# Kernel tuning notes

Hardware: AMD Instinct MI355X
Metric: run time of the kernel (lower is better)

The kernel has to match this reference:

```python
import jax, jax.numpy as jnp
import numpy as np

SEQ = 2048
D_MODEL = 1024
N_HEADS = 16
TOP_K = 64
Q_LR = 128
KV_LR = 128
ROPE_DIM = 32
V_DIM = 64
IDX_DIM = 64
# Mamba2 indexer block: expand=1, headdim=32, d_state=64, d_conv=4
D_INNER = D_MODEL
M_HD = 32
M_NH = D_INNER // M_HD  # 32 ssm heads
M_DS = 64
M_DC = 4
CONV_CH = D_INNER + 2 * M_DS  # 1152
IN_DIM = 2 * D_INNER + 2 * M_DS + M_NH  # 2208


def _silu(x):
    return x * jax.nn.sigmoid(x)


def _mamba2(x, in_w, conv_w, conv_b, dt_bias, A_log, D, norm_w, out_w):
    # Minimal Mamba2 (SSD) recurrent forward: in_proj -> causal depthwise conv
    # on (x, B, C) -> selective scan with scalar-per-head A -> gated RMSNorm -> out_proj.
    L = x.shape[0]
    zxbcdt = x @ in_w.T  # [L, IN_DIM]
    z = zxbcdt[:, :D_INNER]
    xBC = zxbcdt[:, D_INNER:D_INNER + CONV_CH]
    dt = zxbcdt[:, -M_NH:]
    # causal depthwise conv1d, kernel M_DC
    xp = jnp.pad(xBC, ((M_DC - 1, 0), (0, 0)))
    conv = conv_b
    for k in range(M_DC):
        conv = conv + xp[k:k + L] * conv_w[:, k]
    xBC = _silu(conv)
    xs = xBC[:, :D_INNER].reshape(L, M_NH, M_HD)          # [L,h,p]
    B = xBC[:, D_INNER:D_INNER + M_DS]                     # [L,n]
    C = xBC[:, D_INNER + M_DS:]                            # [L,n]
    dt = jax.nn.softplus(dt + dt_bias)                     # [L,h]
    dA = jnp.exp(dt * (-jnp.exp(A_log)))                   # [L,h]
    dBx = jnp.einsum('lh,lhp,ln->lhpn', dt, xs, B)         # [L,h,p,n]

    def step(h, inp):
        dA_t, dBx_t, C_t = inp
        h = h * dA_t[:, None, None] + dBx_t
        y_t = jnp.einsum('hpn,n->hp', h, C_t)
        return h, y_t

    h0 = jnp.zeros((M_NH, M_HD, M_DS), x.dtype)
    _, y = jax.lax.scan(step, h0, (dA, dBx, C))            # y: [L,h,p]
    y = y + D[:, None] * xs
    y = y.reshape(L, D_INNER) * _silu(z)                   # gated
    y = y * jax.lax.rsqrt(jnp.mean(y * y, axis=-1, keepdims=True) + 1e-5) * norm_w
    return y @ out_w.T


def _make_rope(L):
    inv = 1.0 / (10000.0 ** (jnp.arange(0, ROPE_DIM, 2, dtype=jnp.float32) / ROPE_DIM))
    ang = jnp.arange(L, dtype=jnp.float32)[:, None] * inv  # [L, ROPE/2]
    return jnp.sin(ang), jnp.cos(ang)


def _apply_rope(x, sin, cos):
    # x: [L, H, ROPE_DIM]; rotate-half convention
    x1, x2 = jnp.split(x, 2, axis=-1)
    s = sin[:, None, :]
    c = cos[:, None, :]
    return jnp.concatenate([x1 * c - x2 * s, x1 * s + x2 * c], axis=-1)


def _forward(x, idx_in_w, idx_conv_w, idx_conv_b, idx_dt_bias, idx_A_log, idx_D,
             idx_norm_w, idx_out_w, idx_q_w, idx_k_w, q_down_w, q_up_w, q_rope_w,
             kv_down_w, kv_up_w, k_rope_w, out_w):
    L = x.shape[0]
    # --- Mamba2 indexer scores ---
    x_mamba = _mamba2(x, idx_in_w, idx_conv_w, idx_conv_b, idx_dt_bias,
                      idx_A_log, idx_D, idx_norm_w, idx_out_w)
    q_idx = x_mamba @ idx_q_w.T                            # [L, IDX_DIM]
    k_idx = x @ idx_k_w.T                                  # [L, IDX_DIM]
    scores = (q_idx @ k_idx.T) * (IDX_DIM ** -0.5)         # [L, L]
    mask = jnp.tril(jnp.ones((L, L), dtype=bool))
    scores = jnp.where(mask, scores, -jnp.inf)
    k_val = min(TOP_K, L)
    _, indices = jax.lax.top_k(scores, k_val)              # [L, K]
    # --- MLA low-rank projections ---
    c_q = x @ q_down_w.T                                   # [L, Q_LR]
    q_content = (c_q @ q_up_w.T).reshape(L, N_HEADS, V_DIM)
    q_rope = (c_q @ q_rope_w.T).reshape(L, N_HEADS, ROPE_DIM)
    c_kv = x @ kv_down_w.T                                 # [L, KV_LR]
    kv = c_kv @ kv_up_w.T                                  # [L, 2*H*V]
    k_content_flat, v_flat = jnp.split(kv, 2, axis=-1)
    k_content = k_content_flat.reshape(L, N_HEADS, V_DIM)
    v = v_flat.reshape(L, N_HEADS, V_DIM)
    k_rope_shared = (x @ k_rope_w.T)[:, None, :]           # [L, 1, ROPE]
    sin, cos = _make_rope(L)
    q_rope_rot = _apply_rope(q_rope, sin, cos)
    k_rope_rot = jnp.tile(_apply_rope(k_rope_shared, sin, cos), (1, N_HEADS, 1))
    q_final = jnp.concatenate([q_content, q_rope_rot], axis=-1)  # [L,H,dk]
    k_final = jnp.concatenate([k_content, k_rope_rot], axis=-1)  # [L,H,dk]
    # --- top-k gather sparse attention ---
    k_sparse = k_final[indices]                            # [L,K,H,dk]
    v_sparse = v[indices]                                  # [L,K,H,dv]
    dk = k_final.shape[-1]
    logits = jnp.einsum('lhd,lkhd->lhk', q_final, k_sparse) * (dk ** -0.5)
    w = jax.nn.softmax(logits, axis=-1)
    attn = jnp.einsum('lhk,lkhd->lhd', w, v_sparse).reshape(L, N_HEADS * V_DIM)
    return attn @ out_w.T


def setup_inputs() -> dict:
    key = jax.random.key(0)
    ks = jax.random.split(key, 16)

    def g(k, shape, s=0.02):
        return jax.random.normal(k, shape, jnp.float32) * s

    return {
        "x": jax.random.normal(ks[0], (SEQ, D_MODEL), jnp.float32),
        "idx_in_w": g(ks[1], (IN_DIM, D_MODEL)),
        "idx_conv_w": g(ks[2], (CONV_CH, M_DC), 0.2),
        "idx_conv_b": jnp.zeros((CONV_CH,), jnp.float32),
        "idx_dt_bias": g(ks[3], (M_NH,), 0.1),
        "idx_A_log": jnp.log(jnp.arange(1, M_NH + 1, dtype=jnp.float32)),
        "idx_D": jnp.ones((M_NH,), jnp.float32),
        "idx_norm_w": jnp.ones((D_INNER,), jnp.float32),
        "idx_out_w": g(ks[4], (D_MODEL, D_INNER)),
        "idx_q_w": g(ks[5], (IDX_DIM, D_MODEL)),
        "idx_k_w": g(ks[6], (IDX_DIM, D_MODEL)),
        "q_down_w": g(ks[7], (Q_LR, D_MODEL)),
        "q_up_w": g(ks[8], (N_HEADS * V_DIM, Q_LR)),
        "q_rope_w": g(ks[9], (N_HEADS * ROPE_DIM, Q_LR)),
        "kv_down_w": g(ks[10], (KV_LR, D_MODEL)),
        "kv_up_w": g(ks[11], (2 * N_HEADS * V_DIM, KV_LR)),
        "k_rope_w": g(ks[12], (ROPE_DIM, D_MODEL)),
        "out_w": g(ks[13], (D_MODEL, N_HEADS * V_DIM)),
    }


def reference(x, idx_in_w, idx_conv_w, idx_conv_b, idx_dt_bias, idx_A_log, idx_D,
              idx_norm_w, idx_out_w, idx_q_w, idx_k_w, q_down_w, q_up_w, q_rope_w,
              kv_down_w, kv_up_w, k_rope_w, out_w):
    return _forward(x, idx_in_w, idx_conv_w, idx_conv_b, idx_dt_bias, idx_A_log,
                    idx_D, idx_norm_w, idx_out_w, idx_q_w, idx_k_w, q_down_w,
                    q_up_w, q_rope_w, kv_down_w, kv_up_w, k_rope_w, out_w)
```

## Files before the change

### kernel.cpp

```cpp
#include <hip/hip_runtime.h>
#include <math.h>

constexpr int L      = 2048;
constexpr int NH     = 16;
constexpr int DINNER = 1024;
constexpr int MNH    = 32;
constexpr int CONVCH = 1152;
constexpr int INDIMP = 2304;
constexpr int CHUNK  = 64;
constexpr int NCH    = 32;

using bf16x8 = __attribute__((ext_vector_type(8))) short;
using f32x4  = __attribute__((ext_vector_type(4))) float;

__device__ __forceinline__ f32x4 splat4(float x) { return (f32x4){x, x, x, x}; }

__device__ __forceinline__ unsigned short f2bf(float f) {
  unsigned u = __float_as_uint(f);
  return (unsigned short)((u + 0x7fffu + ((u >> 16) & 1u)) >> 16);
}
__device__ __forceinline__ float bf2f(unsigned short h) {
  return __uint_as_float((unsigned)h << 16);
}

__global__ __launch_bounds__(256) void gemm_f32_v3(
    const float* __restrict__ A, const float* __restrict__ W,
    float* __restrict__ C, int M, int N, int K, int tri) {
  __shared__ float As[16][132];
  __shared__ float Ws[16][132];
  int tid = threadIdx.x;
  int bm = blockIdx.y * 128, bn = blockIdx.x * 128;
  if (tri && bn > bm + 127) return;
  int kper = K / gridDim.z;
  int kb = blockIdx.z * kper, ke = kb + kper;
  int lr = tid >> 1;
  int lh = (tid & 1) * 8;
  int tx = tid & 15, ty = tid >> 4;
  bool wok = (bn + lr < N);
  const float* arow = A + (size_t)(bm + lr) * K + lh;
  const float* wrow = W + (size_t)(bn + lr) * K + lh;
  float4 a0, a1, w0, w1;
  auto gload = [&](int k0) {
    a0 = *(const float4*)(arow + k0);
    a1 = *(const float4*)(arow + k0 + 4);
    w0 = make_float4(0.f, 0.f, 0.f, 0.f); w1 = w0;
    if (wok) {
      w0 = *(const float4*)(wrow + k0);
      w1 = *(const float4*)(wrow + k0 + 4);
    }
  };
  f32x4 acc0[8] = {}, acc1[8] = {};
  gload(kb);
  for (int k0 = kb; k0 < ke; k0 += 16) {
    __syncthreads();
    As[lh+0][lr]=a0.x; As[lh+1][lr]=a0.y; As[lh+2][lr]=a0.z; As[lh+3][lr]=a0.w;
    As[lh+4][lr]=a1.x; As[lh+5][lr]=a1.y; As[lh+6][lr]=a1.z; As[lh+7][lr]=a1.w;
    Ws[lh+0][lr]=w0.x; Ws[lh+1][lr]=w0.y; Ws[lh+2][lr]=w0.z; Ws[lh+3][lr]=w0.w;
    Ws[lh+4][lr]=w1.x; Ws[lh+5][lr]=w1.y; Ws[lh+6][lr]=w1.z; Ws[lh+7][lr]=w1.w;
    __syncthreads();
    if (k0 + 16 < ke) gload(k0 + 16);
#pragma unroll
    for (int kk = 0; kk < 16; ++kk) {
      f32x4 b0 = *(const f32x4*)&Ws[kk][tx * 4];
      f32x4 b1 = *(const f32x4*)&Ws[kk][64 + tx * 4];
      f32x4 al = *(const f32x4*)&As[kk][ty * 8];
      f32x4 ah = *(const f32x4*)&As[kk][ty * 8 + 4];
#pragma unroll
      for (int i = 0; i < 4; ++i) {
        acc0[i]     += splat4(al[i]) * b0;
        acc1[i]     += splat4(al[i]) * b1;
        acc0[i + 4] += splat4(ah[i]) * b0;
        acc1[i + 4] += splat4(ah[i]) * b1;
      }
    }
  }
  bool single = (gridDim.z == 1);
#pragma unroll
  for (int i = 0; i < 8; ++i) {
    int row = bm + ty * 8 + i;
    float* crow = C + (size_t)row * N;
    int c0 = bn + tx * 4, c1 = bn + 64 + tx * 4;
    if (c0 + 3 < N) {
      if (single) *(f32x4*)(crow + c0) = acc0[i];
      else {
        atomicAdd(crow + c0 + 0, acc0[i][0]); atomicAdd(crow + c0 + 1, acc0[i][1]);
        atomicAdd(crow + c0 + 2, acc0[i][2]); atomicAdd(crow + c0 + 3, acc0[i][3]);
      }
    }
    if (c1 + 3 < N) {
      if (single) *(f32x4*)(crow + c1) = acc1[i];
      else {
        atomicAdd(crow + c1 + 0, acc1[i][0]); atomicAdd(crow + c1 + 1, acc1[i][1]);
        atomicAdd(crow + c1 + 2, acc1[i][2]); atomicAdd(crow + c1 + 3, acc1[i][3]);
      }
    }
  }
}

__global__ __launch_bounds__(256) void gemm_f32_dual(
    const float* __restrict__ A0, const float* __restrict__ W0, float* __restrict__ C0,
    const float* __restrict__ A1, const float* __restrict__ W1, float* __restrict__ C1,
    int M, int N, int K, int S) {
  __shared__ float As[16][132];
  __shared__ float Ws[16][132];
  int tid = threadIdx.x;
  int bm = blockIdx.y * 128, bn = blockIdx.x * 128;
  int pair = (int)blockIdx.z >= S;
  int zi = blockIdx.z - pair * S;
  const float* A = pair ? A1 : A0;
  const float* W = pair ? W1 : W0;
  float* C = pair ? C1 : C0;
  int kper = K / S;
  int kb = zi * kper, ke = kb + kper;
  int lr = tid >> 1;
  int lh = (tid & 1) * 8;
  int tx = tid & 15, ty = tid >> 4;
  bool wok = (bn + lr < N);
  const float* arow = A + (size_t)(bm + lr) * K + lh;
  const float* wrow = W + (size_t)(bn + lr) * K + lh;
  float4 a0, a1, w0, w1;
  auto gload = [&](int k0) {
    a0 = *(const float4*)(arow + k0);
    a1 = *(const float4*)(arow + k0 + 4);
    w0 = make_float4(0.f, 0.f, 0.f, 0.f); w1 = w0;
    if (wok) {
      w0 = *(const float4*)(wrow + k0);
      w1 = *(const float4*)(wrow + k0 + 4);
    }
  };
  f32x4 acc0[8] = {}, acc1[8] = {};
  gload(kb);
  for (int k0 = kb; k0 < ke; k0 += 16) {
    __syncthreads();
    As[lh+0][lr]=a0.x; As[lh+1][lr]=a0.y; As[lh+2][lr]=a0.z; As[lh+3][lr]=a0.w;
    As[lh+4][lr]=a1.x; As[lh+5][lr]=a1.y; As[lh+6][lr]=a1.z; As[lh+7][lr]=a1.w;
    Ws[lh+0][lr]=w0.x; Ws[lh+1][lr]=w0.y; Ws[lh+2][lr]=w0.z; Ws[lh+3][lr]=w0.w;
    Ws[lh+4][lr]=w1.x; Ws[lh+5][lr]=w1.y; Ws[lh+6][lr]=w1.z; Ws[lh+7][lr]=w1.w;
    __syncthreads();
    if (k0 + 16 < ke) gload(k0 + 16);
#pragma unroll
    for (int kk = 0; kk < 16; ++kk) {
      f32x4 b0 = *(const f32x4*)&Ws[kk][tx * 4];
      f32x4 b1 = *(const f32x4*)&Ws[kk][64 + tx * 4];
      f32x4 al = *(const f32x4*)&As[kk][ty * 8];
      f32x4 ah = *(const f32x4*)&As[kk][ty * 8 + 4];
#pragma unroll
      for (int i = 0; i < 4; ++i) {
        acc0[i]     += splat4(al[i]) * b0;
        acc1[i]     += splat4(al[i]) * b1;
        acc0[i + 4] += splat4(ah[i]) * b0;
        acc1[i + 4] += splat4(ah[i]) * b1;
      }
    }
  }
#pragma unroll
  for (int i = 0; i < 8; ++i) {
    int row = bm + ty * 8 + i;
    float* crow = C + (size_t)row * N;
    int c0 = bn + tx * 4, c1 = bn + 64 + tx * 4;
    if (c0 + 3 < N) {
      atomicAdd(crow + c0 + 0, acc0[i][0]); atomicAdd(crow + c0 + 1, acc0[i][1]);
      atomicAdd(crow + c0 + 2, acc0[i][2]); atomicAdd(crow + c0 + 3, acc0[i][3]);
    }
    if (c1 + 3 < N) {
      atomicAdd(crow + c1 + 0, acc1[i][0]); atomicAdd(crow + c1 + 1, acc1[i][1]);
      atomicAdd(crow + c1 + 2, acc1[i][2]); atomicAdd(crow + c1 + 3, acc1[i][3]);
    }
  }
}

__global__ __launch_bounds__(256) void transpose1024_kernel(
    const float* __restrict__ src, float* __restrict__ dst) {
  __shared__ float t[32][33];
  int bx = blockIdx.x & 31, by = blockIdx.x >> 5;
  int tx = threadIdx.x & 31, ty8 = threadIdx.x >> 5;
  for (int r = ty8; r < 32; r += 8)
    t[r][tx] = src[(size_t)(by * 32 + r) * 1024 + bx * 32 + tx];
  __syncthreads();
  for (int r = ty8; r < 32; r += 8)
    dst[(size_t)(bx * 32 + r) * 1024 + by * 32 + tx] = t[tx][r];
}

__global__ __launch_bounds__(256) void gemm_bf16_kernel(
    const unsigned short* __restrict__ A, const unsigned short* __restrict__ W,
    float* __restrict__ C, int M, int N, int K, int lda, int ldb, int ldc) {
  __shared__ unsigned short As[2][128 * 64];
  __shared__ unsigned short Ws[2][128 * 64];
  int tid = threadIdx.x;
  int bx = blockIdx.x, by = blockIdx.y;
  int nxy = gridDim.x * gridDim.y;
  if ((nxy & 7) == 0) {
    int lin = by * gridDim.x + bx;
    int cpx = nxy >> 3;
    int swz = (lin & 7) * cpx + (lin >> 3);
    bx = swz % gridDim.x;
    by = swz / gridDim.x;
  }
  int bm = by * 128, bn = bx * 128;
  int kper = K / gridDim.z;
  int k_begin = blockIdx.z * kper;
  int k_end = k_begin + kper;
  int wv = tid >> 6, lane = tid & 63;
  int wrow = (wv >> 1) * 64, wcol = (wv & 1) * 64;
  int lrow = lane & 15, quad = lane >> 4;

  f32x4 acc[4][4] = {};

  auto stage = [&](int b, int k0) {
#pragma unroll
    for (int it = 0; it < 4; ++it) {
      int s = it * 256 + tid;
      int r = s >> 3;
      int q = (s & 7) ^ (r & 7);
      const unsigned short* ga = A + (size_t)(bm + r) * lda + k0 + q * 8;
      const unsigned short* gw = W + (size_t)(bn + r) * ldb + k0 + q * 8;
      __builtin_amdgcn_global_load_lds((const __attribute__((address_space(1))) void*)ga,
                                       (__attribute__((address_space(3))) void*)&As[b][s * 8], 16, 0, 0);
      __builtin_amdgcn_global_load_lds((const __attribute__((address_space(1))) void*)gw,
                                       (__attribute__((address_space(3))) void*)&Ws[b][s * 8], 16, 0, 0);
    }
  };

  stage(0, k_begin);
  int cur = 0;
  for (int k0 = k_begin; k0 < k_end; k0 += 64) {
    __syncthreads();
    if (k0 + 64 < k_end) stage(cur ^ 1, k0 + 64);
#pragma unroll
    for (int ks = 0; ks < 2; ++ks) {
      bf16x8 af[4], wf[4];
#pragma unroll
      for (int i = 0; i < 4; ++i) {
        int ra = wrow + i * 16 + lrow;
        int qa = (ks * 4 + quad) ^ (ra & 7);
        af[i] = *(const bf16x8*)&As[cur][(ra * 8 + qa) * 8];
        int rw = wcol + i * 16 + lrow;
        int qw = (ks * 4 + quad) ^ (rw & 7);
        wf[i] = *(const bf16x8*)&Ws[cur][(rw * 8 + qw) * 8];
      }
#pragma unroll
      for (int i = 0; i < 4; ++i)
#pragma unroll
        for (int j = 0; j < 4; ++j)
          acc[i][j] = __builtin_amdgcn_mfma_f32_16x16x32_bf16(af[i], wf[j], acc[i][j], 0, 0, 0);
    }
    cur ^= 1;
  }
  bool single = (gridDim.z == 1);
#pragma unroll
  for (int i = 0; i < 4; ++i)
#pragma unroll
    for (int j = 0; j < 4; ++j)
#pragma unroll
      for (int r = 0; r < 4; ++r) {
        int row = bm + wrow + i * 16 + quad * 4 + r;
        int col = bn + wcol + j * 16 + lrow;
        float v = acc[i][j][r];
        if (single) C[(size_t)row * ldc + col] = v;
        else atomicAdd(&C[(size_t)row * ldc + col], v);
      }
}

__global__ __launch_bounds__(256) void gemm_bf16_dual(
    const unsigned short* __restrict__ A0, const unsigned short* __restrict__ W0,
    float* __restrict__ C0,
    const unsigned short* __restrict__ A1, const unsigned short* __restrict__ W1,
    float* __restrict__ C1,
    int nx0, int ldc0, int ldc1, int K, int ld) {
  __shared__ unsigned short As[2][128 * 64];
  __shared__ unsigned short Ws[2][128 * 64];
  int tid = threadIdx.x;
  int bx = blockIdx.x, by = blockIdx.y;
  int pair = bx >= nx0;
  int bxl = pair ? bx - nx0 : bx;
  const unsigned short* A = pair ? A1 : A0;
  const unsigned short* W = pair ? W1 : W0;
  float* C = pair ? C1 : C0;
  int ldc = pair ? ldc1 : ldc0;
  int bm = by * 128, bn = bxl * 128;
  int wv = tid >> 6, lane = tid & 63;
  int wrow = (wv >> 1) * 64, wcol = (wv & 1) * 64;
  int lrow = lane & 15, quad = lane >> 4;

  f32x4 acc[4][4] = {};

  auto stage = [&](int b, int k0) {
#pragma unroll
    for (int it = 0; it < 4; ++it) {
      int s = it * 256 + tid;
      int r = s >> 3;
      int q = (s & 7) ^ (r & 7);
      const unsigned short* ga = A + (size_t)(bm + r) * ld + k0 + q * 8;
      const unsigned short* gw = W + (size_t)(bn + r) * ld + k0 + q * 8;
      __builtin_amdgcn_global_load_lds((const __attribute__((address_space(1))) void*)ga,
                                       (__attribute__((address_space(3))) void*)&As[b][s * 8], 16, 0, 0);
      __builtin_amdgcn_global_load_lds((const __attribute__((address_space(1))) void*)gw,
                                       (__attribute__((address_space(3))) void*)&Ws[b][s * 8], 16, 0, 0);
    }
  };

  stage(0, 0);
  int cur = 0;
  for (int k0 = 0; k0 < K; k0 += 64) {
    __syncthreads();
    if (k0 + 64 < K) stage(cur ^ 1, k0 + 64);
#pragma unroll
    for (int ks = 0; ks < 2; ++ks) {
      bf16x8 af[4], wf[4];
#pragma unroll
      for (int i = 0; i < 4; ++i) {
        int ra = wrow + i * 16 + lrow;
        int qa = (ks * 4 + quad) ^ (ra & 7);
        af[i] = *(const bf16x8*)&As[cur][(ra * 8 + qa) * 8];
        int rw = wcol + i * 16 + lrow;
        int qw = (ks * 4 + quad) ^ (rw & 7);
        wf[i] = *(const bf16x8*)&Ws[cur][(rw * 8 + qw) * 8];
      }
#pragma unroll
      for (int i = 0; i < 4; ++i)
#pragma unroll
        for (int j = 0; j < 4; ++j)
          acc[i][j] = __builtin_amdgcn_mfma_f32_16x16x32_bf16(af[i], wf[j], acc[i][j], 0, 0, 0);
    }
    cur ^= 1;
  }
#pragma unroll
  for (int i = 0; i < 4; ++i)
#pragma unroll
    for (int j = 0; j < 4; ++j)
#pragma unroll
      for (int r = 0; r < 4; ++r) {
        int row = bm + wrow + i * 16 + quad * 4 + r;
        int col = bn + wcol + j * 16 + lrow;
        C[(size_t)row * ldc + col] = acc[i][j][r];
      }
}

__global__ __launch_bounds__(256) void prep_weights_kernel(
    const float* __restrict__ x, unsigned short* __restrict__ x_trip,
    const float* __restrict__ idx_in_w, unsigned short* __restrict__ w_in_trip,
    const float* __restrict__ q_down_w, const float* __restrict__ kv_down_w,
    const float* __restrict__ k_rope_w, unsigned short* __restrict__ w3down,
    const float* __restrict__ q_up_w, const float* __restrict__ q_rope_w,
    unsigned short* __restrict__ wqups,
    const float* __restrict__ kv_up_w, unsigned short* __restrict__ wkvup) {
  int i = blockIdx.x * 256 + threadIdx.x;
  if (i < 2097152) {
    float f = x[i];
    unsigned short h = f2bf(f);
    float r1 = f - bf2f(h);
    unsigned short m = f2bf(r1);
    unsigned short l = f2bf(r1 - bf2f(m));
    size_t o = (size_t)i * 6;
    x_trip[o] = h; x_trip[o + 1] = m; x_trip[o + 2] = l;
    x_trip[o + 3] = h; x_trip[o + 4] = m; x_trip[o + 5] = h;
  } else if (i < 4456448) {
    int j = i - 2097152;
    int n = j >> 10, k = j & 1023;
    unsigned short h = 0, m = 0, l = 0;
    if (n < 2208) {
      float f = idx_in_w[(size_t)n * 1024 + k];
      h = f2bf(f);
      float r1 = f - bf2f(h);
      m = f2bf(r1);
      l = f2bf(r1 - bf2f(m));
    }
    size_t o = (size_t)j * 6;
    w_in_trip[o] = h; w_in_trip[o + 1] = h; w_in_trip[o + 2] = h;
    w_in_trip[o + 3] = m; w_in_trip[o + 4] = m; w_in_trip[o + 5] = l;
  } else {
    int j2 = i - 4456448;
    const float* src; unsigned short* dst; int rows, K; size_t obase; int idx;
    if (j2 < 393216) {
      int r = j2 >> 17;
      idx = j2 & 131071;
      K = 1024;
      src = (r == 0) ? q_down_w : (r == 1) ? kv_down_w : k_rope_w;
      rows = (r == 2) ? 32 : 128;
      dst = w3down; obase = (size_t)(r * 131072 + idx) * 3;
    } else if (j2 < 524288) {
      idx = j2 - 393216; K = 128; src = q_up_w; rows = 1024;
      dst = wqups; obase = (size_t)idx * 3;
    } else if (j2 < 589824) {
      idx = j2 - 524288; K = 128; src = q_rope_w; rows = 512;
      dst = wqups; obase = (size_t)393216 + (size_t)idx * 3;
    } else {
      idx = j2 - 589824; K = 128; src = kv_up_w; rows = 2048;
      dst = wkvup; obase = (size_t)idx * 3;
    }
    int n = idx / K, k = idx - n * K;
    unsigned short hi = 0, lo = 0;
    if (n < rows) {
      float f = src[(size_t)n * K + k];
      hi = f2bf(f);
      lo = f2bf(f - bf2f(hi));
    }
    dst[obase] = hi; dst[obase + 1] = hi; dst[obase + 2] = lo;
  }
}

__global__ __launch_bounds__(256) void post_inproj_kernel(
    const float* __restrict__ out_w, unsigned short* __restrict__ w_outp,
    const float* __restrict__ zxbcdt, const float* __restrict__ conv_w,
    const float* __restrict__ conv_b, float* __restrict__ xBC,
    const float* __restrict__ dt_bias, const float* __restrict__ A_log,
    float* __restrict__ dt, float* __restrict__ logdA) {
  int i = blockIdx.x * 256 + threadIdx.x;
  if (i < 1048576) {
    float f = out_w[i];
    unsigned short hi = f2bf(f);
    unsigned short lo = f2bf(f - bf2f(hi));
    size_t o = (size_t)i * 3;
    w_outp[o] = hi; w_outp[o + 1] = hi; w_outp[o + 2] = lo;
  } else if (i < 3407872) {
    int idx = i - 1048576;
    int l = idx / CONVCH, c = idx - l * CONVCH;
    float acc = conv_b[c];
#pragma unroll
    for (int k = 0; k < 4; ++k) {
      int ls = l - 3 + k;
      if (ls >= 0) acc += zxbcdt[(size_t)ls * INDIMP + DINNER + c] * conv_w[c * 4 + k];
    }
    xBC[idx] = acc / (1.f + expf(-acc));
  } else {
    int idx = i - 3407872;
    int l = idx >> 5, h = idx & 31;
    float xv = zxbcdt[(size_t)l * INDIMP + 2176 + h] + dt_bias[h];
    float sp = fmaxf(xv, 0.f) + log1pf(expf(-fabsf(xv)));
    dt[idx] = sp;
    logdA[idx] = sp * -expf(A_log[h]);
  }
}

__global__ __launch_bounds__(256) void conv_augA_kernel(
    const float* __restrict__ src, unsigned short* __restrict__ dst,
    int total, int K, int sld) {
  int i = blockIdx.x * 256 + threadIdx.x;
  if (i >= total) return;
  int m = i / K, k = i - m * K;
  float f = src[(size_t)m * sld + k];
  unsigned short hi = f2bf(f);
  unsigned short lo = f2bf(f - bf2f(hi));
  size_t o = ((size_t)m * K + k) * 3;
  dst[o] = hi; dst[o + 1] = lo; dst[o + 2] = hi;
}
__global__ __launch_bounds__(256) void conv_augA2_kernel(
    const float* __restrict__ c3, unsigned short* __restrict__ dq,
    unsigned short* __restrict__ dkv) {
  int i = blockIdx.x * 256 + threadIdx.x;
  if (i >= 2048 * 256) return;
  int m = i >> 8, k = i & 255;
  float f = c3[(size_t)m * 384 + k];
  unsigned short hi = f2bf(f);
  unsigned short lo = f2bf(f - bf2f(hi));
  if (k < 128) {
    size_t o = ((size_t)m * 128 + k) * 3;
    dq[o] = hi; dq[o + 1] = lo; dq[o + 2] = hi;
  } else {
    size_t o = ((size_t)m * 128 + (k - 128)) * 3;
    dkv[o] = hi; dkv[o + 1] = lo; dkv[o + 2] = hi;
  }
}

__global__ __launch_bounds__(256) void lcd_kernel(
    const float* __restrict__ logdA, float* __restrict__ lcd) {
  int i = blockIdx.x * 256 + threadIdx.x;
  if (i >= NCH * MNH) return;
  int c = i >> 5, h = i & 31;
  float s = 0.f;
  for (int t = 0; t < CHUNK; ++t) {
    s += logdA[(c * CHUNK + t) * MNH + h];
    lcd[(size_t)i * CHUNK + t] = s;
  }
}

__global__ __launch_bounds__(256) void chunk_G_kernel(
    const float* __restrict__ xBC, float* __restrict__ G) {
  int c = blockIdx.x, tid = threadIdx.x;
  __shared__ float BsT[64][68];
  __shared__ float Cs[64][65];
  int t = tid >> 2, q = tid & 3;
  const float* row = xBC + (size_t)(c * 64 + t) * CONVCH + DINNER;
#pragma unroll
  for (int j = 0; j < 16; j += 4) {
    float4 b = *(const float4*)(row + q * 16 + j);
    BsT[q * 16 + j + 0][t] = b.x; BsT[q * 16 + j + 1][t] = b.y;
    BsT[q * 16 + j + 2][t] = b.z; BsT[q * 16 + j + 3][t] = b.w;
    float4 cv = *(const float4*)(row + 64 + q * 16 + j);
    Cs[t][q * 16 + j + 0] = cv.x; Cs[t][q * 16 + j + 1] = cv.y;
    Cs[t][q * 16 + j + 2] = cv.z; Cs[t][q * 16 + j + 3] = cv.w;
  }
  __syncthreads();
  int s0 = q * 16;
  f32x4 g0 = {}, g1 = {}, g2 = {}, g3 = {};
  for (int n = 0; n < 64; ++n) {
    f32x4 cv = splat4(Cs[t][n]);
    g0 += cv * *(const f32x4*)&BsT[n][s0];
    g1 += cv * *(const f32x4*)&BsT[n][s0 + 4];
    g2 += cv * *(const f32x4*)&BsT[n][s0 + 8];
    g3 += cv * *(const f32x4*)&BsT[n][s0 + 12];
  }
  float* gp = G + ((size_t)c * 64 + t) * 64 + s0;
  *(f32x4*)gp = g0; *(f32x4*)(gp + 4) = g1; *(f32x4*)(gp + 8) = g2; *(f32x4*)(gp + 12) = g3;
}

__global__ __launch_bounds__(256) void scan_local_kernel(
    const float* __restrict__ xBC, const float* __restrict__ dt,
    const float* __restrict__ lcd, float* __restrict__ hstate) {
  int c = blockIdx.x >> 5, h = blockIdx.x & 31;
  int tid = threadIdx.x;
  __shared__ float Bs[64][68];
  __shared__ float xss[64][36];
  __shared__ float w2s[64];
  int t0 = c * CHUNK;
  int t = tid >> 2, q = tid & 3;
  const float* row = xBC + (size_t)(t0 + t) * CONVCH;
#pragma unroll
  for (int j = 0; j < 16; j += 4)
    *(float4*)&Bs[t][q * 16 + j] = *(const float4*)(row + DINNER + q * 16 + j);
  if (q < 2) {
#pragma unroll
    for (int j = 0; j < 16; j += 4)
      *(float4*)&xss[t][q * 16 + j] = *(const float4*)(row + h * 32 + q * 16 + j);
  }
  if (tid < 64) {
    const float* lc = lcd + ((size_t)c * 32 + h) * CHUNK;
    w2s[tid] = expf(lc[63] - lc[tid]) * dt[(t0 + tid) * MNH + h];
  }
  __syncthreads();
  int n = tid >> 2, pg = (tid & 3) * 8;
  f32x4 h0 = {}, h1 = {};
  for (int s = 0; s < 64; ++s) {
    f32x4 wb = splat4(w2s[s] * Bs[s][n]);
    h0 += wb * *(const f32x4*)&xss[s][pg];
    h1 += wb * *(const f32x4*)&xss[s][pg + 4];
  }
  float* hp = hstate + ((size_t)c * 32 + h) * 2048 + n * 32 + pg;
  *(f32x4*)hp = h0; *(f32x4*)(hp + 4) = h1;
}

__global__ __launch_bounds__(256) void scan_combine_kernel(
    float* __restrict__ hstate, const float* __restrict__ lcd) {
  int i = blockIdx.x * 256 + threadIdx.x;
  int h = i >> 11;
  float H = 0.f;
  for (int c = 0; c < NCH; ++c) {
    float hl = hstate[(size_t)c * 65536 + i];
    hstate[(size_t)c * 65536 + i] = H;
    float P = expf(lcd[((size_t)c * 32 + h) * CHUNK + CHUNK - 1]);
    H = H * P + hl;
  }
}

__global__ __launch_bounds__(256) void scan_y_kernel(
    const float* __restrict__ xBC, const float* __restrict__ G,
    const float* __restrict__ dt, const float* __restrict__ lcd,
    const float* __restrict__ hstate, float* __restrict__ y) {
  int c = blockIdx.x >> 5, h = blockIdx.x & 31;
  int tid = threadIdx.x;
  __shared__ float Ms[64][65];
  __shared__ float Cs[64][65];
  __shared__ float xss[64][36];
  __shared__ float Hss[64][36];
  __shared__ float lcds[64], dts[64];
  int t0 = c * CHUNK;
  int t = tid >> 2, q = tid & 3;
  const float* row = xBC + (size_t)(t0 + t) * CONVCH;
#pragma unroll
  for (int j = 0; j < 16; j += 4) {
    float4 cv = *(const float4*)(row + DINNER + 64 + q * 16 + j);
    Cs[t][q * 16 + j + 0] = cv.x; Cs[t][q * 16 + j + 1] = cv.y;
    Cs[t][q * 16 + j + 2] = cv.z; Cs[t][q * 16 + j + 3] = cv.w;
  }
  if (q < 2) {
#pragma unroll
    for (int j = 0; j < 16; j += 4)
      *(float4*)&xss[t][q * 16 + j] = *(const float4*)(row + h * 32 + q * 16 + j);
  }
  {
    const float* gp = G + ((size_t)c * 64 + t) * 64 + q * 16;
#pragma unroll
    for (int j = 0; j < 16; j += 4) {
      float4 g = *(const float4*)(gp + j);
      Ms[t][q * 16 + j + 0] = g.x; Ms[t][q * 16 + j + 1] = g.y;
      Ms[t][q * 16 + j + 2] = g.z; Ms[t][q * 16 + j + 3] = g.w;
    }
  }
  {
    const float* hp = hstate + ((size_t)c * 32 + h) * 2048 + tid * 8;
    int n = tid >> 2, p0 = (tid & 3) * 8;
    *(float4*)&Hss[n][p0]     = *(const float4*)hp;
    *(float4*)&Hss[n][p0 + 4] = *(const float4*)(hp + 4);
  }
  if (tid < 64) {
    lcds[tid] = lcd[((size_t)c * 32 + h) * CHUNK + tid];
    dts[tid]  = dt[(t0 + tid) * MNH + h];
  }
  __syncthreads();
  {
    int s0 = q * 16;
#pragma unroll
    for (int j = 0; j < 16; ++j) {
      int s = s0 + j;
      float m = (s <= t) ? expf(lcds[t] - lcds[s]) * dts[s] * Ms[t][s] : 0.f;
      Ms[t][s] = m;
    }
  }
  __syncthreads();
  int pg = q * 8;
  f32x4 y0 = {}, y1 = {}, a0 = {}, a1 = {};
  for (int s = 0; s < 64; ++s) {
    f32x4 m = splat4(Ms[t][s]);
    y0 += m * *(const f32x4*)&xss[s][pg];
    y1 += m * *(const f32x4*)&xss[s][pg + 4];
  }
  for (int n = 0; n < 64; ++n) {
    f32x4 cn = splat4(Cs[t][n]);
    a0 += cn * *(const f32x4*)&Hss[n][pg];
    a1 += cn * *(const f32x4*)&Hss[n][pg + 4];
  }
  f32x4 cd = splat4(expf(lcds[t]));
  y0 += cd * a0; y1 += cd * a1;
  float* yp = y + (size_t)(t0 + t) * DINNER + h * 32 + pg;
  *(f32x4*)yp = y0; *(f32x4*)(yp + 4) = y1;
}

__global__ __launch_bounds__(256) void gatenorm_kernel(
    const float* __restrict__ y_ssm, const float* __restrict__ xBC,
    const float* __restrict__ zxbcdt, const float* __restrict__ Dv,
    const float* __restrict__ norm_w, float* __restrict__ out) {
  int l = blockIdx.x, tid = threadIdx.x;
  float vals[4];
  float ss = 0.f;
#pragma unroll
  for (int i = 0; i < 4; ++i) {
    int d = tid + i * 256;
    int h = d >> 5;
    float v = y_ssm[(size_t)l * DINNER + d] + Dv[h] * xBC[(size_t)l * CONVCH + d];
    float z = zxbcdt[(size_t)l * INDIMP + d];
    v *= z / (1.f + expf(-z));
    vals[i] = v;
    ss += v * v;
  }
#pragma unroll
  for (int off = 32; off > 0; off >>= 1) ss += __shfl_xor(ss, off);
  __shared__ float sred[4];
  if ((tid & 63) == 0) sred[tid >> 6] = ss;
  __syncthreads();
  float tot = sred[0] + sred[1] + sred[2] + sred[3];
  float scale = rsqrtf(tot * (1.f / 1024.f) + 1e-5f);
#pragma unroll
  for (int i = 0; i < 4; ++i) {
    int d = tid + i * 256;
    out[(size_t)l * DINNER + d] = vals[i] * scale * norm_w[d];
  }
}

__global__ __launch_bounds__(256) void topk_kernel(
    const float* __restrict__ scores, int* __restrict__ out_idx) {
  int l = blockIdx.x, tid = threadIdx.x;
  if (l < 64) {
    if (tid < 64) out_idx[l * 64 + tid] = tid;
    return;
  }
  int n = l + 1;
  const float* row = scores + (size_t)l * L;
  __shared__ int hist[256];
  __shared__ unsigned sel_prefix;
  __shared__ int sel_remaining;
  __shared__ int cnt_g, cnt_e;
  __shared__ int eq_list[128];
  if (tid == 0) { cnt_g = 0; cnt_e = 0; }
  unsigned prefix = 0;
  int remaining = 64;
  for (int pass = 0; pass < 4; ++pass) {
    int shift = 24 - 8 * pass;
    unsigned himask = (pass == 0) ? 0u : (0xFFFFFFFFu << (shift + 8));
    hist[tid] = 0;
    __syncthreads();
    for (int j = tid; j < n; j += 256) {
      unsigned u = __float_as_uint(row[j]);
      unsigned key = (u & 0x80000000u) ? ~u : (u | 0x80000000u);
      if (((key ^ prefix) & himask) == 0)
        atomicAdd(&hist[(key >> shift) & 255], 1);
    }
    __syncthreads();
    if (tid == 0) {
      int cum = 0, b = 255;
      for (; b >= 0; --b) {
        cum += hist[b];
        if (cum >= remaining) break;
      }
      sel_prefix = prefix | ((unsigned)b << shift);
      sel_remaining = remaining - (cum - hist[b]);
    }
    __syncthreads();
    prefix = sel_prefix;
    remaining = sel_remaining;
    __syncthreads();
  }
  unsigned T = prefix;
  for (int j = tid; j < n; j += 256) {
    unsigned u = __float_as_uint(row[j]);
    unsigned key = (u & 0x80000000u) ? ~u : (u | 0x80000000u);
    if (key > T) {
      int p = atomicAdd(&cnt_g, 1);
      out_idx[l * 64 + p] = j;
    } else if (key == T) {
      int p = atomicAdd(&cnt_e, 1);
      if (p < 128) eq_list[p] = j;
    }
  }
  __syncthreads();
  if (tid == 0) {
    int G = cnt_g;
    int E = remaining;
    int m = cnt_e < 128 ? cnt_e : 128;
    for (int e = 0; e < E; ++e) {
      int best = 0, bj = 0x7fffffff;
      for (int i = 0; i < m; ++i)
        if (eq_list[i] < bj) { bj = eq_list[i]; best = i; }
      out_idx[l * 64 + G + e] = bj;
      eq_list[best] = 0x7fffffff;
    }
  }
}

__global__ __launch_bounds__(128) void rope_pack_kernel(
    const float* __restrict__ qbuf, const float* __restrict__ kv,
    const float* __restrict__ c3,
    float* __restrict__ q_final, float* __restrict__ k_final) {
  int l = blockIdx.x, tid = threadIdx.x;
  __shared__ float s_s[16], s_c[16];
  if (tid < 16) {
    float inv = powf(10000.f, -(float)tid / 16.f);
    float ang = (float)l * inv;
    s_s[tid] = sinf(ang);
    s_c[tid] = cosf(ang);
  }
  __syncthreads();
  const float* qrow = qbuf + (size_t)l * 1536;
  const float* krow = c3 + (size_t)l * 384 + 256;
  for (int e = tid; e < NH * 96; e += 128) {
    int hh = e / 96, d = e - hh * 96;
    float qv, kvv;
    if (d < 64) {
      qv  = qrow[hh * 64 + d];
      kvv = kv[(size_t)l * 2048 + hh * 64 + d];
    } else {
      int r = d - 64;
      if (r < 16) {
        float q1 = qrow[1024 + hh * 32 + r];
        float q2 = qrow[1024 + hh * 32 + 16 + r];
        qv = q1 * s_c[r] - q2 * s_s[r];
        float k1 = krow[r];
        float k2 = krow[16 + r];
        kvv = k1 * s_c[r] - k2 * s_s[r];
      } else {
        int rr = r - 16;
        float q1 = qrow[1024 + hh * 32 + rr];
        float q2 = qrow[1024 + hh * 32 + 16 + rr];
        qv = q1 * s_s[rr] + q2 * s_c[rr];
        float k1 = krow[rr];
        float k2 = krow[16 + rr];
        kvv = k1 * s_s[rr] + k2 * s_c[rr];
      }
    }
    q_final[(size_t)l * 1536 + e] = qv;
    k_final[(size_t)l * 1536 + e] = kvv;
  }
}

__global__ __launch_bounds__(256) void attn_kernel(
    const float* __restrict__ q_final, const float* __restrict__ k_final,
    const float* __restrict__ kv, const int* __restrict__ idx,
    unsigned short* __restrict__ attn_aug) {
  int l = blockIdx.x;
  int tid = threadIdx.x;
  int h = tid >> 4;
  int s = tid & 15;
  __shared__ __align__(16) float lg[16][64];
  __shared__ int iks[64];

  if (tid < 64) iks[tid] = idx[l * 64 + tid];

  const float* qrow = q_final + (size_t)l * 1536 + h * 96 + s * 2;
  float q0 = qrow[0],  q1 = qrow[1];
  float q2 = qrow[32], q3 = qrow[33];
  float q4 = qrow[64], q5 = qrow[65];
  __syncthreads();

#pragma unroll 4
  for (int k = 0; k < 64; ++k) {
    const float* kr = k_final + (size_t)iks[k] * 1536 + h * 96 + s * 2;
    float2 a = *(const float2*)kr;
    float2 b = *(const float2*)(kr + 32);
    float2 c = *(const float2*)(kr + 64);
    float d = q0 * a.x + q1 * a.y + q2 * b.x + q3 * b.y + q4 * c.x + q5 * c.y;
    d += __shfl_xor(d, 1);
    d += __shfl_xor(d, 2);
    d += __shfl_xor(d, 4);
    d += __shfl_xor(d, 8);
    if (s == 0) lg[h][k] = d * 0.10206207261596575f;
  }
  __syncthreads();

  f32x4 lv = *(const f32x4*)&lg[h][s * 4];
  float m = fmaxf(fmaxf(lv[0], lv[1]), fmaxf(lv[2], lv[3]));
#pragma unroll
  for (int off = 1; off < 16; off <<= 1) m = fmaxf(m, __shfl_xor(m, off));
  f32x4 ev;
  ev[0] = expf(lv[0] - m); ev[1] = expf(lv[1] - m);
  ev[2] = expf(lv[2] - m); ev[3] = expf(lv[3] - m);
  float ssum = ev[0] + ev[1] + ev[2] + ev[3];
#pragma unroll
  for (int off = 1; off < 16; off <<= 1) ssum += __shfl_xor(ssum, off);
  float inv = 1.f / ssum;
  lg[h][s * 4 + 0] = ev[0] * inv;
  lg[h][s * 4 + 1] = ev[1] * inv;
  lg[h][s * 4 + 2] = ev[2] * inv;
  lg[h][s * 4 + 3] = ev[3] * inv;
  __syncthreads();

  f32x4 acc = {};
#pragma unroll 4
  for (int k = 0; k < 64; ++k) {
    const float* vr = kv + (size_t)iks[k] * 2048 + 1024 + tid * 4;
    f32x4 v = *(const f32x4*)vr;
    acc += splat4(lg[h][k]) * v;
  }

#pragma unroll
  for (int i = 0; i < 4; ++i) {
    float a = acc[i];
    unsigned short hi = f2bf(a);
    unsigned short lo = f2bf(a - bf2f(hi));
    size_t o = ((size_t)l * 1024 + tid * 4 + i) * 3;
    attn_aug[o] = hi; attn_aug[o + 1] = lo; attn_aug[o + 2] = hi;
  }
}

extern "C" void kernel_launch(void* const* d_in, const int* in_sizes, int n_in,
                              void* d_out, int out_size, void* d_ws, size_t ws_size,
                              hipStream_t stream) {
  const float* x          = (const float*)d_in[0];
  const float* idx_in_w   = (const float*)d_in[1];
  const float* idx_conv_w = (const float*)d_in[2];
  const float* idx_conv_b = (const float*)d_in[3];
  const float* idx_dt_b   = (const float*)d_in[4];
  const float* idx_A_log  = (const float*)d_in[5];
  const float* idx_D      = (const float*)d_in[6];
  const float* idx_norm_w = (const float*)d_in[7];
  const float* idx_out_w  = (const float*)d_in[8];
  const float* idx_q_w    = (const float*)d_in[9];
  const float* idx_k_w    = (const float*)d_in[10];
  const float* q_down_w   = (const float*)d_in[11];
  const float* q_up_w     = (const float*)d_in[12];
  const float* q_rope_w   = (const float*)d_in[13];
  const float* kv_down_w  = (const float*)d_in[14];
  const float* kv_up_w    = (const float*)d_in[15];
  const float* k_rope_w   = (const float*)d_in[16];
  const float* out_w      = (const float*)d_in[17];
  float* out = (float*)d_out;

  float* p = (float*)d_ws;
  float* segA = p; p += 4718592;
  float* segB = p; p += 2359296;
  float* dtb = p; p += 65536;
  float* logdA = p; p += 65536;
  float* lcdb = p; p += 65536;
  int*   idxb = (int*)p; p += 131072;
  float* segD = p; p += 4194304;
  float* segBig1 = p; p += 6291456;
  float* segBig2 = p; p += 7077888;
  float* segH = p; p += 3145728;
  unsigned short* w_3down_aug = (unsigned short*)p; p += 589824;
  unsigned short* w_qups_aug  = (unsigned short*)p; p += 294912;
  unsigned short* w_kvup_aug  = (unsigned short*)p; p += 393216;
  unsigned short* c_q_aug     = (unsigned short*)p; p += 393216;
  unsigned short* c_kv_aug    = (unsigned short*)p; p += 393216;
  float* Gbuf = p; p += 131072;

  float* zxbcdt = segA;
  float* scores = segA;
  float* qbuf   = segA;
  float* xBC    = segB;
  float* q_idx  = segB;
  float* k_idx  = segB + 131072;
  float* c3     = segB + 262144;
  float* y_ssm  = segD;
  float* hstate = segD + 2097152;
  float* kvb    = segD;
  unsigned short* x_trip     = (unsigned short*)segBig1;
  unsigned short* w_outp_aug = (unsigned short*)segBig1;
  unsigned short* w_in_trip  = (unsigned short*)segBig2;
  float* y_norm  = segBig2;
  unsigned short* x_aug = (unsigned short*)segBig2;
  float* q_final = segBig2;
  unsigned short* attn_aug = (unsigned short*)(segBig2 + 3145728);
  float* out_w_T = segH;
  float* qwpad   = segH + 1048576;
  float* Wq      = segH + 1179648;
  float* k_final = segH;

  dim3 blk(256);
  auto cdiv = [](int a, int b) { return (a + b - 1) / b; };
  auto gemmf3 = [&](const float* A, const float* W, float* C, int M, int N, int K, int S, int tri) {
    dim3 grid(cdiv(N, 128), M / 128, S);
    hipLaunchKernelGGL(gemm_f32_v3, grid, blk, 0, stream, A, W, C, M, N, K, tri);
  };
  auto gemmb = [&](const unsigned short* A, const unsigned short* W, float* C,
                   int M, int N, int K, int lda, int ldb, int ldc, int S) {
    dim3 grid(N / 128, M / 128, S);
    hipLaunchKernelGGL(gemm_bf16_kernel, grid, blk, 0, stream, A, W, C, M, N, K, lda, ldb, ldc);
  };

  hipLaunchKernelGGL(transpose1024_kernel, dim3(1024), blk, 0, stream, idx_out_w, out_w_T);
  hipMemsetAsync(qwpad, 0, 262144 * 4, stream);
  hipMemcpyAsync(qwpad, idx_q_w, (size_t)64 * 1024 * 4, hipMemcpyDeviceToDevice, stream);
  gemmf3(qwpad, out_w_T, Wq, 128, 1024, 1024, 8, 0);
  hipLaunchKernelGGL(prep_weights_kernel, dim3(20736), blk, 0, stream,
                     x, x_trip, idx_in_w, w_in_trip,
                     q_down_w, kv_down_w, k_rope_w, w_3down_aug,
                     q_up_w, q_rope_w, w_qups_aug, kv_up_w, w_kvup_aug);

  hipMemsetAsync(zxbcdt, 0, (size_t)L * INDIMP * 4, stream);
  gemmb(x_trip, w_in_trip, zxbcdt, 2048, 2304, 6144, 6144, 6144, INDIMP, 4);
  hipLaunchKernelGGL(post_inproj_kernel, dim3(13568), blk, 0, stream,
                     out_w, w_outp_aug, zxbcdt, idx_conv_w, idx_conv_b, xBC,
                     idx_dt_b, idx_A_log, dtb, logdA);
  hipLaunchKernelGGL(lcd_kernel, dim3(4), blk, 0, stream, logdA, lcdb);
  hipLaunchKernelGGL(chunk_G_kernel, dim3(NCH), blk, 0, stream, xBC, Gbuf);
  hipLaunchKernelGGL(scan_local_kernel, dim3(NCH * MNH), blk, 0, stream,
                     xBC, dtb, lcdb, hstate);
  hipLaunchKernelGGL(scan_combine_kernel, dim3(256), blk, 0, stream, hstate, lcdb);
  hipLaunchKernelGGL(scan_y_kernel, dim3(NCH * MNH), blk, 0, stream,
                     xBC, Gbuf, dtb, lcdb, hstate, y_ssm);
  hipLaunchKernelGGL(gatenorm_kernel, dim3(L), blk, 0, stream,
                     y_ssm, xBC, zxbcdt, idx_D, idx_norm_w, y_norm);

  hipMemsetAsync(q_idx, 0, 262144 * 4, stream);
  {
    dim3 grid(1, 16, 32);
    hipLaunchKernelGGL(gemm_f32_dual, grid, blk, 0, stream,
                       y_norm, Wq, q_idx, x, idx_k_w, k_idx, 2048, 64, 1024, 16);
  }
  gemmf3(q_idx, k_idx, scores, 2048, 2048, 64, 1, 1);
  hipLaunchKernelGGL(topk_kernel, dim3(L), blk, 0, stream, scores, idxb);

  hipLaunchKernelGGL(conv_augA_kernel, dim3(cdiv(2048 * 1024, 256)), blk, 0, stream,
                     x, x_aug, 2048 * 1024, 1024, 1024);
  hipMemsetAsync(c3, 0, 786432 * 4, stream);
  gemmb(x_aug, w_3down_aug, c3, 2048, 384, 3072, 3072, 3072, 384, 8);
  hipLaunchKernelGGL(conv_augA2_kernel, dim3(cdiv(2048 * 256, 256)), blk, 0, stream,
                     c3, c_q_aug, c_kv_aug);
  {
    dim3 grid(28, 16, 1);
    hipLaunchKernelGGL(gemm_bf16_dual, grid, blk, 0, stream,
                       c_q_aug, w_qups_aug, qbuf,
                       c_kv_aug, w_kvup_aug, kvb,
                       12, 1536, 2048, 384, 384);
  }
  hipLaunchKernelGGL(rope_pack_kernel, dim3(L), dim3(128), 0, stream,
                     qbuf, kvb, c3, q_final, k_final);

  hipLaunchKernelGGL(attn_kernel, dim3(L), blk, 0, stream,
                     q_final, k_final, kvb, idxb, attn_aug);
  hipMemsetAsync(out, 0, (size_t)out_size * 4, stream);
  gemmb(attn_aug, w_outp_aug, out, 2048, 1024, 3072, 3072, 3072, 1024, 4);
}
```

Measured before the change: 661.5 us.

## Merge small kernels into neighbours, reduce in-proj split-K, swizzle attention block order

The transpose of idx_out_w moves into extra blocks of prep_weights_kernel, and the lcd prefix-sum moves into extra blocks of chunk_G_kernel, which removes two kernel launches. The in-proj bf16 GEMM split-K factor drops from 4 to 2, which halves the atomic or partial traffic but leaves fewer blocks in flight. The attention kernel remaps block index to row with an interleaved order, meant to change cache locality. The merged kernels share block shape, and the transpose blocks bring a __syncthreads into an otherwise elementwise kernel.

```diff
diff --git a/kernel.cpp b/kernel.cpp
--- a/kernel.cpp
+++ b/kernel.cpp
@@ -169,18 +169,6 @@
   }
 }
 
-__global__ __launch_bounds__(256) void transpose1024_kernel(
-    const float* __restrict__ src, float* __restrict__ dst) {
-  __shared__ float t[32][33];
-  int bx = blockIdx.x & 31, by = blockIdx.x >> 5;
-  int tx = threadIdx.x & 31, ty8 = threadIdx.x >> 5;
-  for (int r = ty8; r < 32; r += 8)
-    t[r][tx] = src[(size_t)(by * 32 + r) * 1024 + bx * 32 + tx];
-  __syncthreads();
-  for (int r = ty8; r < 32; r += 8)
-    dst[(size_t)(bx * 32 + r) * 1024 + by * 32 + tx] = t[tx][r];
-}
-
 __global__ __launch_bounds__(256) void gemm_bf16_kernel(
     const unsigned short* __restrict__ A, const unsigned short* __restrict__ W,
     float* __restrict__ C, int M, int N, int K, int lda, int ldb, int ldc) {
@@ -343,8 +331,22 @@
     const float* __restrict__ k_rope_w, unsigned short* __restrict__ w3down,
     const float* __restrict__ q_up_w, const float* __restrict__ q_rope_w,
     unsigned short* __restrict__ wqups,
-    const float* __restrict__ kv_up_w, unsigned short* __restrict__ wkvup) {
-  int i = blockIdx.x * 256 + threadIdx.x;
+    const float* __restrict__ kv_up_w, unsigned short* __restrict__ wkvup,
+    const float* __restrict__ idx_out_w, float* __restrict__ out_w_T) {
+  __shared__ float tsh[32][33];
+  int bid = blockIdx.x;
+  if (bid >= 20736) {
+    int b = bid - 20736;
+    int bx = b & 31, by = b >> 5;
+    int tx = threadIdx.x & 31, ty8 = threadIdx.x >> 5;
+    for (int r = ty8; r < 32; r += 8)
+      tsh[r][tx] = idx_out_w[(size_t)(by * 32 + r) * 1024 + bx * 32 + tx];
+    __syncthreads();
+    for (int r = ty8; r < 32; r += 8)
+      out_w_T[(size_t)(bx * 32 + r) * 1024 + by * 32 + tx] = tsh[tx][r];
+    return;
+  }
+  int i = bid * 256 + threadIdx.x;
   if (i < 2097152) {
     float f = x[i];
     unsigned short h = f2bf(f);
@@ -462,21 +464,20 @@
   }
 }
 
-__global__ __launch_bounds__(256) void lcd_kernel(
+__global__ __launch_bounds__(256) void chunk_G_kernel(
+    const float* __restrict__ xBC, float* __restrict__ G,
     const float* __restrict__ logdA, float* __restrict__ lcd) {
-  int i = blockIdx.x * 256 + threadIdx.x;
-  if (i >= NCH * MNH) return;
-  int c = i >> 5, h = i & 31;
-  float s = 0.f;
-  for (int t = 0; t < CHUNK; ++t) {
-    s += logdA[(c * CHUNK + t) * MNH + h];
-    lcd[(size_t)i * CHUNK + t] = s;
-  }
-}
-
-__global__ __launch_bounds__(256) void chunk_G_kernel(
-    const float* __restrict__ xBC, float* __restrict__ G) {
   int c = blockIdx.x, tid = threadIdx.x;
+  if (c >= NCH) {
+    int i = (c - NCH) * 256 + tid;
+    int cc = i >> 5, h = i & 31;
+    float s = 0.f;
+    for (int t = 0; t < CHUNK; ++t) {
+      s += logdA[(cc * CHUNK + t) * MNH + h];
+      lcd[(size_t)i * CHUNK + t] = s;
+    }
+    return;
+  }
   __shared__ float BsT[64][68];
   __shared__ float Cs[64][65];
   int t = tid >> 2, q = tid & 3;
@@ -775,7 +776,8 @@
     const float* __restrict__ q_final, const float* __restrict__ k_final,
     const float* __restrict__ kv, const int* __restrict__ idx,
     unsigned short* __restrict__ attn_aug) {
-  int l = blockIdx.x;
+  int b = blockIdx.x;
+  int l = (b & 7) * 256 + (b >> 3);
   int tid = threadIdx.x;
   int h = tid >> 4;
   int s = tid & 15;
@@ -794,9 +796,9 @@
   for (int k = 0; k < 64; ++k) {
     const float* kr = k_final + (size_t)iks[k] * 1536 + h * 96 + s * 2;
     float2 a = *(const float2*)kr;
-    float2 b = *(const float2*)(kr + 32);
+    float2 b2 = *(const float2*)(kr + 32);
     float2 c = *(const float2*)(kr + 64);
-    float d = q0 * a.x + q1 * a.y + q2 * b.x + q3 * b.y + q4 * c.x + q5 * c.y;
+    float d = q0 * a.x + q1 * a.y + q2 * b2.x + q3 * b2.y + q4 * c.x + q5 * c.y;
     d += __shfl_xor(d, 1);
     d += __shfl_xor(d, 2);
     d += __shfl_xor(d, 4);
@@ -915,22 +917,22 @@
     hipLaunchKernelGGL(gemm_bf16_kernel, grid, blk, 0, stream, A, W, C, M, N, K, lda, ldb, ldc);
   };
 
-  hipLaunchKernelGGL(transpose1024_kernel, dim3(1024), blk, 0, stream, idx_out_w, out_w_T);
+  hipLaunchKernelGGL(prep_weights_kernel, dim3(21760), blk, 0, stream,
+                     x, x_trip, idx_in_w, w_in_trip,
+                     q_down_w, kv_down_w, k_rope_w, w_3down_aug,
+                     q_up_w, q_rope_w, w_qups_aug, kv_up_w, w_kvup_aug,
+                     idx_out_w, out_w_T);
   hipMemsetAsync(qwpad, 0, 262144 * 4, stream);
   hipMemcpyAsync(qwpad, idx_q_w, (size_t)64 * 1024 * 4, hipMemcpyDeviceToDevice, stream);
   gemmf3(qwpad, out_w_T, Wq, 128, 1024, 1024, 8, 0);
-  hipLaunchKernelGGL(prep_weights_kernel, dim3(20736), blk, 0, stream,
-                     x, x_trip, idx_in_w, w_in_trip,
-                     q_down_w, kv_down_w, k_rope_w, w_3down_aug,
-                     q_up_w, q_rope_w, w_qups_aug, kv_up_w, w_kvup_aug);
 
   hipMemsetAsync(zxbcdt, 0, (size_t)L * INDIMP * 4, stream);
-  gemmb(x_trip, w_in_trip, zxbcdt, 2048, 2304, 6144, 6144, 6144, INDIMP, 4);
+  gemmb(x_trip, w_in_trip, zxbcdt, 2048, 2304, 6144, 6144, 6144, INDIMP, 2);
   hipLaunchKernelGGL(post_inproj_kernel, dim3(13568), blk, 0, stream,
                      out_w, w_outp_aug, zxbcdt, idx_conv_w, idx_conv_b, xBC,
                      idx_dt_b, idx_A_log, dtb, logdA);
-  hipLaunchKernelGGL(lcd_kernel, dim3(4), blk, 0, stream, logdA, lcdb);
-  hipLaunchKernelGGL(chunk_G_kernel, dim3(NCH), blk, 0, stream, xBC, Gbuf);
+  hipLaunchKernelGGL(chunk_G_kernel, dim3(NCH + 4), blk, 0, stream,
+                     xBC, Gbuf, logdA, lcdb);
   hipLaunchKernelGGL(scan_local_kernel, dim3(NCH * MNH), blk, 0, stream,
                      xBC, dtb, lcdb, hstate);
   hipLaunchKernelGGL(scan_combine_kernel, dim3(256), blk, 0, stream, hstate, lcdb);
```

New measurement: 645.8 us. 1.02x faster.
